# Kernel tuning notes

Measured on AMD Instinct MI355X. Metric: run time of the kernel, lower is better.

The kernel has to match this reference:

```python
import jax, jax.numpy as jnp
import numpy as np

LN_EPS = 1e-5
BN_EPS = 1e-5


def setup_inputs() -> dict:
    key = jax.random.key(0)
    k0, k1, k2, k3 = jax.random.split(key, 4)
    N, C, T, V, S = 128, 64, 128, 25, 3  # batch, channels, frames, joints, subsets
    rel = C // 8                          # rel_channels = 8
    inner = rel * S                       # hidden_dim * n_heads = 24
    x = jax.random.normal(k0, (N, C, T, V), dtype=jnp.float32)
    # graph adjacency parameter (3 subsets over 25 joints); small positive values
    PA = jax.random.uniform(k1, (S, V, V), dtype=jnp.float32) * 0.1
    ln_gamma = jnp.ones((C,), jnp.float32)
    ln_beta = jnp.zeros((C,), jnp.float32)
    # to_qk: Linear(C, 2*inner), weight init normal(0, 1) per source
    Wqk = jax.random.normal(k2, (2 * inner, C), dtype=jnp.float32)
    bqk = jnp.zeros((2 * inner,), jnp.float32)
    # conv_branch_init: normal(0, sqrt(2/(out*1*1*branches)))
    conv_w = jax.random.normal(k3, (S, C, C), dtype=jnp.float32) * np.float32(np.sqrt(2.0 / (C * S)))
    conv_b = jnp.zeros((S, C), jnp.float32)
    bn_gamma = jnp.ones((C,), jnp.float32)
    bn_beta = jnp.zeros((C,), jnp.float32)
    bn_mean = jnp.zeros((C,), jnp.float32)
    bn_var = jnp.ones((C,), jnp.float32)
    return {"x": x, "PA": PA, "ln_gamma": ln_gamma, "ln_beta": ln_beta,
            "Wqk": Wqk, "bqk": bqk, "conv_w": conv_w, "conv_b": conv_b,
            "bn_gamma": bn_gamma, "bn_beta": bn_beta, "bn_mean": bn_mean, "bn_var": bn_var}


def reference(x, PA, ln_gamma, ln_beta, Wqk, bqk, conv_w, conv_b,
              bn_gamma, bn_beta, bn_mean, bn_var):
    N, C, T, V = x.shape
    S = PA.shape[0]                       # num_subset == n_heads
    rel = Wqk.shape[0] // (2 * S)         # hidden dim per head
    scale = rel ** (-0.5)

    xv = jnp.transpose(x, (0, 2, 3, 1))   # n t v c

    # --- SelfAttention: LayerNorm -> Linear -> per-head softmax(q k^T) ---
    mu = jnp.mean(xv, axis=-1, keepdims=True)
    var = jnp.mean(jnp.square(xv - mu), axis=-1, keepdims=True)
    yn = (xv - mu) * jax.lax.rsqrt(var + LN_EPS) * ln_gamma + ln_beta
    qk = yn @ Wqk.T + bqk                 # n t v (2*inner)
    inner = qk.shape[-1] // 2
    q = qk[..., :inner].reshape(N, T, V, S, rel)
    k = qk[..., inner:].reshape(N, T, V, S, rel)
    dots = jnp.einsum('ntihd,ntjhd->nthij', q, k) * scale  # (n,t,h,V,V)
    attn = jax.nn.softmax(dots, axis=-1)

    # --- attention-modulated adjacency + per-subset aggregation ---
    A = attn * PA[None, None]             # (n,t,h,V,V)
    z = jnp.einsum('nthij,ntjc->nthic', A, xv)  # (n,t,h,V,C) messages per subset
    # per-subset 1x1 conv then sum over subsets
    out = jnp.einsum('nthvc,hoc->notv', z, conv_w) \
        + jnp.sum(conv_b, axis=0)[None, :, None, None]  # (n,C,t,V)

    # --- BatchNorm2d (eval-mode with provided stats) + residual + ReLU ---
    bn_out = (out - bn_mean[None, :, None, None]) \
        * jax.lax.rsqrt(bn_var + BN_EPS)[None, :, None, None] \
        * bn_gamma[None, :, None, None] + bn_beta[None, :, None, None]
    return jax.nn.relu(bn_out + x)        # down is identity since in_c == out_c
```

## Files before the change

### kernel.cpp

```cpp
#include <hip/hip_runtime.h>
#include <hip/hip_bf16.h>
#include <math.h>

typedef __attribute__((ext_vector_type(8))) short bf16x8;
typedef __attribute__((ext_vector_type(4))) float f32x4;

__device__ inline unsigned short f2bf(float f) {
    return __builtin_bit_cast(unsigned short, __float2bfloat16(f));
}
__device__ inline float bf2f(unsigned short u) {
    return __bfloat162float(__builtin_bit_cast(__hip_bfloat16, u));
}
__device__ inline bf16x8 cvt8(float4 a, float4 b) {
    bf16x8 r;
    r[0]=(short)f2bf(a.x); r[1]=(short)f2bf(a.y); r[2]=(short)f2bf(a.z); r[3]=(short)f2bf(a.w);
    r[4]=(short)f2bf(b.x); r[5]=(short)f2bf(b.y); r[6]=(short)f2bf(b.z); r[7]=(short)f2bf(b.w);
    return r;
}
__device__ inline void split8(float4 a, float4 b, bf16x8& hi, bf16x8& lo) {
    float f[8] = {a.x,a.y,a.z,a.w,b.x,b.y,b.z,b.w};
    #pragma unroll
    for (int i = 0; i < 8; ++i) {
        unsigned short h = f2bf(f[i]);
        hi[i] = (short)h;
        lo[i] = (short)f2bf(f[i] - bf2f(h));
    }
}

#define LDS_FLOATS 7532

__global__ __launch_bounds__(256, 5)
void agcn_fused_kernel(const float* __restrict__ x,
                       const float* __restrict__ PA,
                       const float* __restrict__ ln_g, const float* __restrict__ ln_b,
                       const float* __restrict__ Wqk, const float* __restrict__ bqk,
                       const float* __restrict__ conv_w, const float* __restrict__ conv_b,
                       const float* __restrict__ bn_g, const float* __restrict__ bn_b,
                       const float* __restrict__ bn_m, const float* __restrict__ bn_v,
                       float* __restrict__ out)
{
    __shared__ float lds[LDS_FLOATS];
    float* xv = lds;
    unsigned short* yn_hi = (unsigned short*)(lds + 1628);
    unsigned short* yn_lo = (unsigned short*)(lds + 2652);
    unsigned short* A_bf  = (unsigned short*)(lds + 1628);
    float* qkb  = lds + 3676;
    unsigned short* xvT = (unsigned short*)(lds + 3676);
    float* Abuf = lds + 5032;
    unsigned short* zA  = (unsigned short*)(lds + 5032);

    const int bid = blockIdx.x;
    const int n = bid >> 7, t = bid & 127;
    const int tid = threadIdx.x;
    const int lane = tid & 63, w = tid >> 6;
    const int g = lane >> 4, l15 = lane & 15;

    const int o = 16 * w + l15;
    float4 cw_f[12];
    #pragma unroll
    for (int kt = 0; kt < 6; ++kt) {
        const float* wp = &conv_w[(kt >> 1) * 4096 + o * 64 + (kt & 1) * 32 + 8 * g];
        cw_f[2*kt]   = *(const float4*)wp;
        cw_f[2*kt+1] = *(const float4*)(wp + 4);
    }
    float4 wq_f[4];
    float bq = 0.f;
    if (w < 3) {
        const int j = 16 * w + l15;
        #pragma unroll
        for (int ks = 0; ks < 2; ++ks) {
            const float* wp = &Wqk[j * 64 + ks * 32 + 8 * g];
            wq_f[2*ks]   = *(const float4*)wp;
            wq_f[2*ks+1] = *(const float4*)(wp + 4);
        }
        bq = bqk[j];
    }

    const float* xbase = x + (size_t)n * 204800 + t * 25;
    for (int idx = tid; idx < 1600; idx += 256) {
        int c = idx / 25, v = idx - c * 25;
        xv[v * 65 + c] = xbase[c * 3200 + v];
    }

    bf16x8 cw[6];
    #pragma unroll
    for (int kt = 0; kt < 6; ++kt) cw[kt] = cvt8(cw_f[2*kt], cw_f[2*kt+1]);
    bf16x8 wqh[2], wql[2];
    if (w < 3) {
        #pragma unroll
        for (int ks = 0; ks < 2; ++ks) split8(wq_f[2*ks], wq_f[2*ks+1], wqh[ks], wql[ks]);
    }
    __syncthreads();

    {
        float lg = ln_g[lane], lb = ln_b[lane];
        for (int v = w; v < 25; v += 4) {
            float val = xv[v * 65 + lane];
            float s = val;
            for (int off = 32; off; off >>= 1) s += __shfl_xor(s, off);
            float mu = s * (1.0f / 64.0f);
            float d = val - mu;
            float s2 = d * d;
            for (int off = 32; off; off >>= 1) s2 += __shfl_xor(s2, off);
            float rstd = rsqrtf(s2 * (1.0f / 64.0f) + 1e-5f);
            float y = d * rstd * lg + lb;
            unsigned short h = f2bf(y);
            unsigned short l = f2bf(y - bf2f(h));
            int idx = (v * 64 + lane) ^ ((v & 7) << 3);
            yn_hi[idx] = h;
            yn_lo[idx] = l;
        }
    }
    __syncthreads();

    if (w < 3) {
        const int j = 16 * w + l15;
        #pragma unroll
        for (int mt = 0; mt < 2; ++mt) {
            f32x4 acc = {bq, bq, bq, bq};
            #pragma unroll
            for (int ks = 0; ks < 2; ++ks) {
                int row = 16 * mt + l15;
                int idx = (row * 64 + ks * 32 + 8 * g) ^ ((row & 7) << 3);
                bf16x8 ah = *(bf16x8*)&yn_hi[idx];
                bf16x8 al = *(bf16x8*)&yn_lo[idx];
                acc = __builtin_amdgcn_mfma_f32_16x16x32_bf16(al, wqh[ks], acc, 0, 0, 0);
                acc = __builtin_amdgcn_mfma_f32_16x16x32_bf16(ah, wql[ks], acc, 0, 0, 0);
                acc = __builtin_amdgcn_mfma_f32_16x16x32_bf16(ah, wqh[ks], acc, 0, 0, 0);
            }
            #pragma unroll
            for (int reg = 0; reg < 4; ++reg) {
                int v = 16 * mt + 4 * g + reg;
                if (v < 25) qkb[v * 52 + j] = acc[reg];
            }
        }
    }
    __syncthreads();

    for (int idx = tid; idx < 1875; idx += 256) {
        int h = idx / 625, r = idx - h * 625;
        int i = r / 25, j = r - i * 25;
        const float4* q = (const float4*)&qkb[i * 52 + h * 8];
        const float4* k = (const float4*)&qkb[j * 52 + 24 + h * 8];
        float4 q0 = q[0], q1 = q[1], k0 = k[0], k1 = k[1];
        float d = q0.x*k0.x + q0.y*k0.y + q0.z*k0.z + q0.w*k0.w
                + q1.x*k1.x + q1.y*k1.y + q1.z*k1.z + q1.w*k1.w;
        Abuf[idx] = d * 0.35355339059327373f;
    }
    __syncthreads();

    if (tid < 75) {
        int h = tid / 25, i = tid - h * 25;
        const float* row = &Abuf[h * 625 + i * 25];
        const float* pa = &PA[h * 625 + i * 25];
        float m = row[0];
        #pragma unroll
        for (int j = 1; j < 25; ++j) m = fmaxf(m, row[j]);
        float e[25];
        float s = 0.f;
        #pragma unroll
        for (int j = 0; j < 25; ++j) { e[j] = __expf(row[j] - m); s += e[j]; }
        float inv = 1.0f / s;
        unsigned short* ar = &A_bf[(h * 25 + i) * 40];
        #pragma unroll
        for (int j = 0; j < 25; ++j) ar[j] = f2bf(e[j] * inv * pa[j]);
        #pragma unroll
        for (int j = 25; j < 32; ++j) ar[j] = 0;
    }
    for (int idx = tid; idx < 2560; idx += 256) {
        int c = idx / 40, j = idx - c * 40;
        float val = (j < 25) ? xv[j * 65 + c] : 0.f;
        xvT[idx] = f2bf(val);
    }
    __syncthreads();

    {
        bf16x8 bfrag = *(bf16x8*)&xvT[(16 * w + l15) * 40 + 8 * g];
        #pragma unroll
        for (int mt = 0; mt < 5; ++mt) {
            bf16x8 afrag = *(bf16x8*)&A_bf[(16 * mt + l15) * 40 + 8 * g];
            f32x4 zacc = {0.f, 0.f, 0.f, 0.f};
            zacc = __builtin_amdgcn_mfma_f32_16x16x32_bf16(afrag, bfrag, zacc, 0, 0, 0);
            #pragma unroll
            for (int reg = 0; reg < 4; ++reg) {
                int r = 16 * mt + 4 * g + reg;
                if (r < 75) {
                    int h = r / 25, i = r - h * 25;
                    zA[i * 200 + h * 64 + 16 * w + l15] = f2bf(zacc[reg]);
                }
            }
        }
    }
    __syncthreads();

    {
        float bg = bn_g[o], bv = bn_v[o], bb = bn_b[o], bm = bn_m[o];
        float cb = conv_b[o] + conv_b[64 + o] + conv_b[128 + o];

        const int r1 = (16 + l15 < 25) ? (16 + l15) : 0;
        f32x4 acc0 = {0.f, 0.f, 0.f, 0.f}, acc1 = {0.f, 0.f, 0.f, 0.f};
        #pragma unroll
        for (int kt = 0; kt < 6; ++kt) {
            bf16x8 a0 = *(bf16x8*)&zA[l15 * 200 + 32 * kt + 8 * g];
            bf16x8 a1 = *(bf16x8*)&zA[r1 * 200 + 32 * kt + 8 * g];
            acc0 = __builtin_amdgcn_mfma_f32_16x16x32_bf16(a0, cw[kt], acc0, 0, 0, 0);
            acc1 = __builtin_amdgcn_mfma_f32_16x16x32_bf16(a1, cw[kt], acc1, 0, 0, 0);
        }
        float sc = bg * rsqrtf(bv + 1e-5f);
        float bi = cb * sc + bb - bm * sc;
        float* ob = out + (size_t)n * 204800 + (size_t)o * 3200 + t * 25;
        #pragma unroll
        for (int reg = 0; reg < 4; ++reg) {
            int v = 4 * g + reg;
            float val = acc0[reg] * sc + bi + xv[v * 65 + o];
            ob[v] = fmaxf(val, 0.f);
        }
        #pragma unroll
        for (int reg = 0; reg < 4; ++reg) {
            int v = 16 + 4 * g + reg;
            if (v < 25) {
                float val = acc1[reg] * sc + bi + xv[v * 65 + o];
                ob[v] = fmaxf(val, 0.f);
            }
        }
    }
}

extern "C" void kernel_launch(void* const* d_in, const int* in_sizes, int n_in,
                              void* d_out, int out_size, void* d_ws, size_t ws_size,
                              hipStream_t stream) {
    const float* x      = (const float*)d_in[0];
    const float* PA     = (const float*)d_in[1];
    const float* ln_g   = (const float*)d_in[2];
    const float* ln_b   = (const float*)d_in[3];
    const float* Wqk    = (const float*)d_in[4];
    const float* bqk    = (const float*)d_in[5];
    const float* conv_w = (const float*)d_in[6];
    const float* conv_b = (const float*)d_in[7];
    const float* bn_g   = (const float*)d_in[8];
    const float* bn_b   = (const float*)d_in[9];
    const float* bn_m   = (const float*)d_in[10];
    const float* bn_v   = (const float*)d_in[11];
    float* outp = (float*)d_out;

    agcn_fused_kernel<<<dim3(128 * 128), dim3(256), 0, stream>>>(
        x, PA, ln_g, ln_b, Wqk, bqk, conv_w, conv_b,
        bn_g, bn_b, bn_m, bn_v, outp);
}
```

Before: 248.3 us.

## Shrink LDS footprint, remap block order, and stage output through shared memory

Compacts the LDS layout by aliasing zA onto the yn/A region and placing the result buffer in the freed space, then raises the launch bound from 5 to 6 blocks per CU. It permutes the block index so consecutive blocks touch different batch/time slices, which changes the DRAM access pattern. The z MFMA results are held in registers across an extra barrier so the zA aliasing stays safe. Outputs are written to LDS first and then stored with a thread-strided loop over channel and joint. The extra barriers and LDS round trip add latency per block in exchange for higher occupancy and more regular stores.

```diff
diff --git a/kernel.cpp b/kernel.cpp
--- a/kernel.cpp
+++ b/kernel.cpp
@@ -27,9 +27,9 @@
     }
 }
 
-#define LDS_FLOATS 7532
-
-__global__ __launch_bounds__(256, 5)
+#define LDS_FLOATS 6403
+
+__global__ __launch_bounds__(256, 6)
 void agcn_fused_kernel(const float* __restrict__ x,
                        const float* __restrict__ PA,
                        const float* __restrict__ ln_g, const float* __restrict__ ln_b,
@@ -41,16 +41,18 @@
 {
     __shared__ float lds[LDS_FLOATS];
     float* xv = lds;
-    unsigned short* yn_hi = (unsigned short*)(lds + 1628);
-    unsigned short* yn_lo = (unsigned short*)(lds + 2652);
-    unsigned short* A_bf  = (unsigned short*)(lds + 1628);
-    float* qkb  = lds + 3676;
-    unsigned short* xvT = (unsigned short*)(lds + 3676);
-    float* Abuf = lds + 5032;
-    unsigned short* zA  = (unsigned short*)(lds + 5032);
+    unsigned short* ynh = (unsigned short*)(lds + 1628);
+    unsigned short* ynl = (unsigned short*)(lds + 2428);
+    unsigned short* A_bf = (unsigned short*)(lds + 1628);
+    float* qkb  = lds + 3228;
+    unsigned short* xvT = (unsigned short*)(lds + 3228);
+    float* Abuf = lds + 4528;
+    unsigned short* zA  = (unsigned short*)(lds + 1628);
+    float* res  = lds + 4528;
 
     const int bid = blockIdx.x;
-    const int n = bid >> 7, t = bid & 127;
+    const int sid = ((bid & 7) << 11) | (bid >> 3);
+    const int n = sid >> 7, t = sid & 127;
     const int tid = threadIdx.x;
     const int lane = tid & 63, w = tid >> 6;
     const int g = lane >> 4, l15 = lane & 15;
@@ -107,8 +109,8 @@
             unsigned short h = f2bf(y);
             unsigned short l = f2bf(y - bf2f(h));
             int idx = (v * 64 + lane) ^ ((v & 7) << 3);
-            yn_hi[idx] = h;
-            yn_lo[idx] = l;
+            ynh[idx] = h;
+            ynl[idx] = l;
         }
     }
     __syncthreads();
@@ -122,8 +124,8 @@
             for (int ks = 0; ks < 2; ++ks) {
                 int row = 16 * mt + l15;
                 int idx = (row * 64 + ks * 32 + 8 * g) ^ ((row & 7) << 3);
-                bf16x8 ah = *(bf16x8*)&yn_hi[idx];
-                bf16x8 al = *(bf16x8*)&yn_lo[idx];
+                bf16x8 ah = *(bf16x8*)&ynh[idx];
+                bf16x8 al = *(bf16x8*)&ynl[idx];
                 acc = __builtin_amdgcn_mfma_f32_16x16x32_bf16(al, wqh[ks], acc, 0, 0, 0);
                 acc = __builtin_amdgcn_mfma_f32_16x16x32_bf16(ah, wql[ks], acc, 0, 0, 0);
                 acc = __builtin_amdgcn_mfma_f32_16x16x32_bf16(ah, wqh[ks], acc, 0, 0, 0);
@@ -174,20 +176,26 @@
     }
     __syncthreads();
 
+    f32x4 zacc[5];
     {
         bf16x8 bfrag = *(bf16x8*)&xvT[(16 * w + l15) * 40 + 8 * g];
         #pragma unroll
         for (int mt = 0; mt < 5; ++mt) {
             bf16x8 afrag = *(bf16x8*)&A_bf[(16 * mt + l15) * 40 + 8 * g];
-            f32x4 zacc = {0.f, 0.f, 0.f, 0.f};
-            zacc = __builtin_amdgcn_mfma_f32_16x16x32_bf16(afrag, bfrag, zacc, 0, 0, 0);
-            #pragma unroll
-            for (int reg = 0; reg < 4; ++reg) {
-                int r = 16 * mt + 4 * g + reg;
-                if (r < 75) {
-                    int h = r / 25, i = r - h * 25;
-                    zA[i * 200 + h * 64 + 16 * w + l15] = f2bf(zacc[reg]);
-                }
+            f32x4 a = {0.f, 0.f, 0.f, 0.f};
+            zacc[mt] = __builtin_amdgcn_mfma_f32_16x16x32_bf16(afrag, bfrag, a, 0, 0, 0);
+        }
+    }
+    __syncthreads();
+
+    #pragma unroll
+    for (int mt = 0; mt < 5; ++mt) {
+        #pragma unroll
+        for (int reg = 0; reg < 4; ++reg) {
+            int r = 16 * mt + 4 * g + reg;
+            if (r < 75) {
+                int h = r / 25, i = r - h * 25;
+                zA[i * 200 + h * 64 + 16 * w + l15] = f2bf(zacc[mt][reg]);
             }
         }
     }
@@ -208,20 +216,28 @@
         }
         float sc = bg * rsqrtf(bv + 1e-5f);
         float bi = cb * sc + bb - bm * sc;
-        float* ob = out + (size_t)n * 204800 + (size_t)o * 3200 + t * 25;
         #pragma unroll
         for (int reg = 0; reg < 4; ++reg) {
             int v = 4 * g + reg;
             float val = acc0[reg] * sc + bi + xv[v * 65 + o];
-            ob[v] = fmaxf(val, 0.f);
+            res[o * 25 + v] = fmaxf(val, 0.f);
         }
         #pragma unroll
         for (int reg = 0; reg < 4; ++reg) {
             int v = 16 + 4 * g + reg;
             if (v < 25) {
                 float val = acc1[reg] * sc + bi + xv[v * 65 + o];
-                ob[v] = fmaxf(val, 0.f);
-            }
+                res[o * 25 + v] = fmaxf(val, 0.f);
+            }
+        }
+    }
+    __syncthreads();
+
+    {
+        float* ob = out + (size_t)n * 204800 + t * 25;
+        for (int idx = tid; idx < 1600; idx += 256) {
+            int c = idx / 25, v = idx - c * 25;
+            ob[c * 3200 + v] = res[idx];
         }
     }
 }
```

Measured after the change: 248.0 us. Within noise of the previous version (-0.1%).
